# Performance work log

Hardware: AMD Instinct MI355X
Metric: run time of the kernel (lower is better)

Reference implementation:

```python
import jax, jax.numpy as jnp
import numpy as np

HIDDEN = 2048
N_EXPERTS = 64
TOP_K = 2
N_TOKENS = 16384


def setup_inputs() -> dict:
    key = jax.random.key(0)
    k1, k2 = jax.random.split(key)
    x = jax.random.normal(k1, (N_TOKENS, HIDDEN), dtype=jnp.float32)
    gate_w = jax.random.normal(k2, (N_EXPERTS, HIDDEN), dtype=jnp.float32) * (1.0 / np.sqrt(HIDDEN))
    gate_b = jnp.zeros((N_EXPERTS,), dtype=jnp.float32)
    return {"x": x, "gate_w": gate_w, "gate_b": gate_b}


def reference(x, gate_w, gate_b):
    # gate: [N, H] @ [H, E] + [E] -> [N, E]
    router_logits = jnp.einsum("nh,eh->ne", x, gate_w) + gate_b
    # softmax over experts in fp32 (matches F.softmax(..., dim=1, dtype=float32))
    router_probs = jax.nn.softmax(router_logits.astype(jnp.float32), axis=1)
    # top-k experts per token
    router_weights, selected_experts_indices = jax.lax.top_k(router_probs, TOP_K)  # [N, K]
    router_weights = router_weights / jnp.sum(router_weights, axis=-1, keepdims=True)
    router_weights = router_weights.astype(x.dtype)
    # one-hot [N, K, E] -> permute(2,1,0) -> [E, K, N]
    expert_mask = jax.nn.one_hot(selected_experts_indices, N_EXPERTS, dtype=jnp.int64 if jax.config.jax_enable_x64 else jnp.int32)
    expert_mask = jnp.transpose(expert_mask, (2, 1, 0))
    return (router_logits, router_weights, selected_experts_indices, expert_mask)
```

## Files before the change

kernel.cpp:

```cpp
#include <hip/hip_runtime.h>
#include <hip/hip_bf16.h>
#include <math.h>

#define HIDDEN 2048
#define NEXP   64
#define NTOK   16384

typedef __attribute__((ext_vector_type(8))) _Float16 f16x8;
typedef __attribute__((ext_vector_type(4))) float   f32x4;

__device__ __forceinline__ void split2_f16(float4 f0, float4 f1, f16x8& h, f16x8& l) {
    float e[8] = {f0.x, f0.y, f0.z, f0.w, f1.x, f1.y, f1.z, f1.w};
    f16x8 hv, lv;
#pragma unroll
    for (int i = 0; i < 8; ++i) {
        _Float16 hh = (_Float16)e[i];
        float r = e[i] - (float)hh;
        hv[i] = hh;
        lv[i] = (_Float16)r;
    }
    h = hv; l = lv;
}

__global__ __launch_bounds__(256) void prep_kernel(
    const float* __restrict__ gw, uint4* __restrict__ wh, uint4* __restrict__ wl)
{
    const int gid = blockIdx.x * 256 + threadIdx.x;
    const int c   = gid >> 9;
    const int e   = (gid >> 3) & 63;
    const int kgp = gid & 7;
    const int kg  = kgp ^ (e & 7);
    const float* src = gw + (size_t)e * HIDDEN + c * 64 + kg * 8;
    float4 s0 = *(const float4*)src;
    float4 s1 = *(const float4*)(src + 4);
    f16x8 h, l;
    split2_f16(s0, s1, h, l);
    wh[gid] = __builtin_bit_cast(uint4, h);
    wl[gid] = __builtin_bit_cast(uint4, l);
}

#define STAGE(cg, bo)                                                                     \
    _Pragma("unroll")                                                                     \
    for (int rr = 0; rr < 2; ++rr) {                                                      \
        const int s = rr * 256 + tid;                                                     \
        __builtin_amdgcn_global_load_lds(                                                 \
            (const __attribute__((address_space(1))) void*)(wh + (size_t)(cg) * 512 + s), \
            (__attribute__((address_space(3))) void*)&Bs[(bo) + s], 16, 0, 0);            \
        __builtin_amdgcn_global_load_lds(                                                 \
            (const __attribute__((address_space(1))) void*)(wl + (size_t)(cg) * 512 + s), \
            (__attribute__((address_space(3))) void*)&Bs[(bo) + 512 + s], 16, 0, 0);      \
    }

__global__ __launch_bounds__(256, 2) void fused_kernel(
    const float* __restrict__ x,
    const uint4* __restrict__ wh,
    const uint4* __restrict__ wl,
    const float* __restrict__ bias_g,
    float* __restrict__ logits,
    float* __restrict__ weights,
    float* __restrict__ idxf,
    float* __restrict__ mask)
{
    __shared__ uint4 Bs[2 * 1024];
    __shared__ float Ls[32][65];
    __shared__ int selA[32], selB[32];

    const int tid = threadIdx.x;
    const int l   = tid & 63;
    const int wv  = tid >> 6;
    const int tg  = wv & 1;
    const int eh  = wv >> 1;
    const int tb0 = blockIdx.x * 32;
    const int t0  = tb0 + tg * 16;

    const float4* xp = (const float4*)(x + (size_t)(t0 + (l & 15)) * HIDDEN) + ((l >> 4) * 2);

    const int lb = ((l & 15) << 3) | ((l >> 4) ^ (l & 7));

    f32x4 acc1[2], acc2[2];
#pragma unroll
    for (int eg = 0; eg < 2; ++eg) {
        acc1[eg] = (f32x4){0.f, 0.f, 0.f, 0.f};
        acc2[eg] = (f32x4){0.f, 0.f, 0.f, 0.f};
    }

    STAGE(0, 0)
    float4 a0 = xp[0], a1 = xp[1], a2 = xp[8], a3 = xp[9];
    __syncthreads();

    const int nch = HIDDEN / 64;
    for (int c = 0; c < nch; ++c) {
        const int buf = c & 1;
        float4 n0 = a0, n1 = a1, n2 = a2, n3 = a3;
        if (c + 1 < nch) {
            STAGE(c + 1, (buf ^ 1) * 1024)
            const int fb = (c + 1) * 16;
            n0 = xp[fb + 0]; n1 = xp[fb + 1]; n2 = xp[fb + 8]; n3 = xp[fb + 9];
        }

#pragma unroll
        for (int ks = 0; ks < 2; ++ks) {
            f16x8 ah, al;
            split2_f16(ks ? a2 : a0, ks ? a3 : a1, ah, al);
            const int ib = buf * 1024 + (lb ^ (ks << 2));
#pragma unroll
            for (int eg = 0; eg < 2; ++eg) {
                const int ego = (eh * 2 + eg) * 128;
                f16x8 bh = __builtin_bit_cast(f16x8, Bs[ib + ego]);
                f16x8 bl = __builtin_bit_cast(f16x8, Bs[ib + 512 + ego]);
                acc1[eg] = __builtin_amdgcn_mfma_f32_16x16x32_f16(ah, bh, acc1[eg], 0, 0, 0);
                acc2[eg] = __builtin_amdgcn_mfma_f32_16x16x32_f16(ah, bl, acc2[eg], 0, 0, 0);
                acc2[eg] = __builtin_amdgcn_mfma_f32_16x16x32_f16(al, bh, acc2[eg], 0, 0, 0);
            }
        }
        a0 = n0; a1 = n1; a2 = n2; a3 = n3;
        __syncthreads();
    }

#pragma unroll
    for (int eg = 0; eg < 2; ++eg) {
        const int col = (eh * 2 + eg) * 16 + (l & 15);
        const float b = bias_g[col];
#pragma unroll
        for (int i = 0; i < 4; ++i)
            Ls[tg * 16 + (l >> 4) * 4 + i][col] = acc1[eg][i] + acc2[eg][i] + b;
    }
    __syncthreads();

#pragma unroll
    for (int i = 0; i < 2; ++i) {
        const int idx = i * 256 + tid;
        const int row = idx >> 4;
        const int c4  = (idx & 15) << 2;
        float4 v;
        v.x = Ls[row][c4 + 0];
        v.y = Ls[row][c4 + 1];
        v.z = Ls[row][c4 + 2];
        v.w = Ls[row][c4 + 3];
        *(float4*)&logits[(size_t)(tb0 + row) * NEXP + c4] = v;
    }

    if (tid < 32) {
        const int t = tid;
        float best = -1e30f, second = -1e30f;
        int bi = 0, si = 0;
#pragma unroll
        for (int e = 0; e < NEXP; ++e) {
            float v = Ls[t][e];
            if (v > best)        { second = best; si = bi; best = v; bi = e; }
            else if (v > second) { second = v; si = e; }
        }
        float r  = __expf(second - best);
        float w0 = 1.f / (1.f + r);
        float w1 = r / (1.f + r);
        const int tgl = tb0 + t;
        weights[2 * tgl + 0] = w0;
        weights[2 * tgl + 1] = w1;
        idxf[2 * tgl + 0] = (float)bi;
        idxf[2 * tgl + 1] = (float)si;
        selA[t] = bi;
        selB[t] = si;
    }
    __syncthreads();

    const int t8 = tid & 7;
    const int pg = tid >> 3;
    const int b0 = 4 * t8;
    int sA0 = selA[b0+0], sA1 = selA[b0+1], sA2 = selA[b0+2], sA3 = selA[b0+3];
    int sB0 = selB[b0+0], sB1 = selB[b0+1], sB2 = selB[b0+2], sB3 = selB[b0+3];
#pragma unroll
    for (int p = 0; p < 4; ++p) {
        const int pair = pg * 4 + p;
        const int e = pair >> 1;
        const int k = pair & 1;
        const int a0 = k ? sB0 : sA0, a1 = k ? sB1 : sA1, a2 = k ? sB2 : sA2, a3 = k ? sB3 : sA3;
        float4 v;
        v.x = (a0 == e) ? 1.f : 0.f;
        v.y = (a1 == e) ? 1.f : 0.f;
        v.z = (a2 == e) ? 1.f : 0.f;
        v.w = (a3 == e) ? 1.f : 0.f;
        *(float4*)&mask[((size_t)e * 2 + k) * NTOK + tb0 + b0] = v;
    }
}

extern "C" void kernel_launch(void* const* d_in, const int* in_sizes, int n_in,
                              void* d_out, int out_size, void* d_ws, size_t ws_size,
                              hipStream_t stream) {
    const float* x  = (const float*)d_in[0];
    const float* gw = (const float*)d_in[1];
    const float* gb = (const float*)d_in[2];

    float* out     = (float*)d_out;
    float* logits  = out;
    float* weights = out + (size_t)NTOK * NEXP;
    float* idxf    = weights + (size_t)NTOK * 2;
    float* mask    = idxf + (size_t)NTOK * 2;

    uint4* wh = (uint4*)d_ws;
    uint4* wl = wh + 16384;

    prep_kernel<<<64, 256, 0, stream>>>(gw, wh, wl);
    fused_kernel<<<NTOK / 32, 256, 0, stream>>>(x, wh, wl, gb, logits, weights, idxf, mask);
}
```

Baseline: 53.76 us.

## Triple-buffer weight staging with explicit vmcnt waits instead of syncthreads

Moves the LDS weight staging from double to triple buffering, so async global-to-LDS loads run two chunks ahead of the MFMA compute. The full __syncthreads is replaced with a partial s_waitcnt vmcnt that waits only for the stage about to be read, followed by a raw s_barrier. The aim is to hide more weight-load latency and avoid draining every outstanding load (including x prefetches) at each iteration. The cost is 16KB more LDS per block and hand-counted vmcnt values that depend on the exact number of issued loads.

Result: slower. 55.33 us (+2.9%).

```diff
diff --git a/kernel.cpp b/kernel.cpp
--- a/kernel.cpp
+++ b/kernel.cpp
@@ -61,7 +61,7 @@
     float* __restrict__ idxf,
     float* __restrict__ mask)
 {
-    __shared__ uint4 Bs[2 * 1024];
+    __shared__ uint4 Bs[3 * 1024];
     __shared__ float Ls[32][65];
     __shared__ int selA[32], selB[32];
 
@@ -86,23 +86,33 @@
 
     STAGE(0, 0)
     float4 a0 = xp[0], a1 = xp[1], a2 = xp[8], a3 = xp[9];
-    __syncthreads();
+    STAGE(1, 1024)
+    asm volatile("s_waitcnt vmcnt(8)" ::: "memory");
+    __builtin_amdgcn_s_barrier();
+    __builtin_amdgcn_sched_barrier(0);
 
     const int nch = HIDDEN / 64;
+    int rd = 0;
+#pragma unroll 1
     for (int c = 0; c < nch; ++c) {
-        const int buf = c & 1;
+        const bool hasA = (c + 1 < nch);
+        const bool hasS = (c + 2 < nch);
+
         float4 n0 = a0, n1 = a1, n2 = a2, n3 = a3;
-        if (c + 1 < nch) {
-            STAGE(c + 1, (buf ^ 1) * 1024)
+        if (hasA) {
             const int fb = (c + 1) * 16;
             n0 = xp[fb + 0]; n1 = xp[fb + 1]; n2 = xp[fb + 8]; n3 = xp[fb + 9];
+        }
+        if (hasS) {
+            const int st = (rd + 2 >= 3) ? (rd - 1) : (rd + 2);
+            STAGE(c + 2, st * 1024)
         }
 
 #pragma unroll
         for (int ks = 0; ks < 2; ++ks) {
             f16x8 ah, al;
             split2_f16(ks ? a2 : a0, ks ? a3 : a1, ah, al);
-            const int ib = buf * 1024 + (lb ^ (ks << 2));
+            const int ib = rd * 1024 + (lb ^ (ks << 2));
 #pragma unroll
             for (int eg = 0; eg < 2; ++eg) {
                 const int ego = (eh * 2 + eg) * 128;
@@ -113,8 +123,19 @@
                 acc2[eg] = __builtin_amdgcn_mfma_f32_16x16x32_f16(al, bh, acc2[eg], 0, 0, 0);
             }
         }
+
+        if (hasS) {
+            asm volatile("s_waitcnt vmcnt(8)" ::: "memory");
+        } else if (hasA) {
+            asm volatile("s_waitcnt vmcnt(4)" ::: "memory");
+        }
+        if (hasA) {
+            __builtin_amdgcn_s_barrier();
+            __builtin_amdgcn_sched_barrier(0);
+        }
+
         a0 = n0; a1 = n1; a2 = n2; a3 = n3;
-        __syncthreads();
+        rd = (rd + 1 >= 3) ? 0 : (rd + 1);
     }
 
 #pragma unroll
```
